# Kernel tuning notes

Hardware: AMD Instinct MI355X
Metric: run time of the kernel (lower is better)

The kernel has to match this reference:

```python
import jax, jax.numpy as jnp
import numpy as np

B, S, IN, H, OUT = 512, 1024, 32, 128, 1


def setup_inputs() -> dict:
    key = jax.random.key(0)
    ks = jax.random.split(key, 7)
    sc = 1.0 / np.sqrt(H)  # torch LSTM/Linear default init scale
    return {
        "x": jax.random.normal(ks[0], (B, S, IN), dtype=jnp.float32),
        "W_ih": jax.random.normal(ks[1], (4 * H, IN), dtype=jnp.float32) * sc,
        "W_hh": jax.random.normal(ks[2], (4 * H, H), dtype=jnp.float32) * sc,
        "b_ih": jax.random.normal(ks[3], (4 * H,), dtype=jnp.float32) * sc,
        "b_hh": jax.random.normal(ks[4], (4 * H,), dtype=jnp.float32) * sc,
        "W_lin": jax.random.normal(ks[5], (OUT, H * S), dtype=jnp.float32) * (1.0 / np.sqrt(H * S)),
        "b_lin": jax.random.normal(ks[6], (OUT,), dtype=jnp.float32) * (1.0 / np.sqrt(H * S)),
    }


def _lstm(x, W_ih, W_hh, b_ih, b_hh):
    # x: [B,S,IN]. Precompute input projection for all timesteps (one big GEMM).
    xw = jnp.einsum("bsi,gi->bsg", x, W_ih) + (b_ih + b_hh)  # [B,S,4H]
    h0 = jnp.zeros((x.shape[0], W_hh.shape[1]), dtype=x.dtype)
    c0 = jnp.zeros_like(h0)

    def step(carry, xw_t):
        h, c = carry
        gates = xw_t + h @ W_hh.T  # [B,4H]
        i, f, g, o = jnp.split(gates, 4, axis=-1)  # torch gate order i,f,g,o
        i = jax.nn.sigmoid(i)
        f = jax.nn.sigmoid(f)
        g = jnp.tanh(g)
        o = jax.nn.sigmoid(o)
        c = f * c + i * g
        h = o * jnp.tanh(c)
        return (h, c), h

    (_, _), hs = jax.lax.scan(step, (h0, c0), jnp.swapaxes(xw, 0, 1))  # hs: [S,B,H]
    return jnp.swapaxes(hs, 0, 1)  # [B,S,H]


def reference(x, W_ih, W_hh, b_ih, b_hh, W_lin, b_lin):
    lstm_out = _lstm(x, W_ih, W_hh, b_ih, b_hh)          # [B,S,H]
    flat = lstm_out.reshape(lstm_out.shape[0], -1)        # [B,S*H]
    return flat @ W_lin.T + b_lin                         # [B,OUT]
```

## Files before the change

### kernel.cpp

```cpp
#include <hip/hip_runtime.h>

constexpr int B = 512, S = 1024, IN = 32, H = 128;
constexpr int KTOT = IN + H;
constexpr int KSL = KTOT / 4;

template <int CTRL>
__device__ __forceinline__ float dpp_qp(float v) {
  return __int_as_float(__builtin_amdgcn_update_dpp(
      0, __float_as_int(v), CTRL, 0xF, 0xF, true));
}
__device__ __forceinline__ float sigm(float v) {
  float e = __builtin_amdgcn_exp2f(-1.4426950408889634f * v);
  return __builtin_amdgcn_rcpf(1.0f + e);
}
__device__ __forceinline__ float tanh_(float v) {
  float e = __builtin_amdgcn_exp2f(-2.8853900817779268f * v);
  return 2.0f * __builtin_amdgcn_rcpf(1.0f + e) - 1.0f;
}

__global__ __launch_bounds__(512, 2)
void lstm_fused(const float* __restrict__ x, const float* __restrict__ Wih,
                const float* __restrict__ Whh, const float* __restrict__ bih,
                const float* __restrict__ bhh, const float* __restrict__ Wlin,
                const float* __restrict__ blin, float* __restrict__ out) {
  __shared__ alignas(16) float hxA[KTOT];
  __shared__ alignas(16) float hxB[KTOT];
  __shared__ float red[2 * H];

  const int tid = threadIdx.x;
  const int g = tid >> 2;
  const int j = tid & 3;
  const int b0 = blockIdx.x * 2;

  float w[4][KSL];
#pragma unroll
  for (int c = 0; c < 4; ++c) {
    const int n = c * H + g;
#pragma unroll
    for (int kk = 0; kk < KSL; ++kk) {
      const int k = KSL * j + kk;
      const float* p = (k < IN) ? (Wih + n * IN + k) : (Whh + n * H + (k - IN));
      w[c][kk] = *p;
    }
  }
  float bias[4];
#pragma unroll
  for (int c = 0; c < 4; ++c) bias[c] = bih[c * H + g] + bhh[c * H + g];

  if (tid < KTOT) { hxA[tid] = 0.0f; hxB[tid] = 0.0f; }
  __syncthreads();
  if (tid < 2 * IN) {
    const int b = tid >> 5, k = tid & 31;
    (b ? hxB : hxA)[k] = x[(size_t)(b0 + b) * (S * IN) + k];
  }
  __syncthreads();

  float cc0 = 0.f, cc1 = 0.f;
  float oa0 = 0.f, oa1 = 0.f;
  const int xb = g >> 5, xk = g & 31;

  for (int s = 0; s < S; ++s) {
    float wl = 0.f, xn = 0.f;
    if (j == 0) wl = Wlin[s * H + g];
    const bool xload = (j == 1) && (g < 64) && (s + 1 < S);
    if (xload) xn = x[(size_t)(b0 + xb) * (S * IN) + (s + 1) * IN + xk];

    float acc[4][2];
#pragma unroll
    for (int c = 0; c < 4; ++c) { acc[c][0] = 0.f; acc[c][1] = 0.f; }
    const float4* pA = reinterpret_cast<const float4*>(hxA + KSL * j);
    const float4* pB = reinterpret_cast<const float4*>(hxB + KSL * j);
#pragma unroll
    for (int q = 0; q < KSL / 4; ++q) {
      const float4 va = pA[q];
      const float4 vb = pB[q];
      const float ea[4] = {va.x, va.y, va.z, va.w};
      const float eb[4] = {vb.x, vb.y, vb.z, vb.w};
#pragma unroll
      for (int u = 0; u < 4; ++u)
#pragma unroll
        for (int c = 0; c < 4; ++c) {
          acc[c][0] = fmaf(ea[u], w[c][4 * q + u], acc[c][0]);
          acc[c][1] = fmaf(eb[u], w[c][4 * q + u], acc[c][1]);
        }
    }
#pragma unroll
    for (int c = 0; c < 4; ++c)
#pragma unroll
      for (int b = 0; b < 2; ++b) {
        float v = acc[c][b];
        v += dpp_qp<0xB1>(v);
        v += dpp_qp<0x4E>(v);
        acc[c][b] = v;
      }
    __syncthreads();
    if (j == 0) {
#pragma unroll
      for (int b = 0; b < 2; ++b) {
        const float gi = sigm(acc[0][b] + bias[0]);
        const float gf = sigm(acc[1][b] + bias[1]);
        const float gc = tanh_(acc[2][b] + bias[2]);
        const float go = sigm(acc[3][b] + bias[3]);
        float& cc = b ? cc1 : cc0;
        cc = gf * cc + gi * gc;
        const float h = go * tanh_(cc);
        (b ? hxB : hxA)[IN + g] = h;
        (b ? oa1 : oa0) += h * wl;
      }
    } else if (xload) {
      (xb ? hxB : hxA)[xk] = xn;
    }
    __syncthreads();
  }

  if (j == 0) { red[2 * g] = oa0; red[2 * g + 1] = oa1; }
  __syncthreads();
  if (tid < 2) {
    float sum = blin[0];
    for (int k = 0; k < H; ++k) sum += red[2 * k + tid];
    out[b0 + tid] = sum;
  }
}

extern "C" void kernel_launch(void* const* d_in, const int* in_sizes, int n_in,
                              void* d_out, int out_size, void* d_ws, size_t ws_size,
                              hipStream_t stream) {
  const float* x    = (const float*)d_in[0];
  const float* Wih  = (const float*)d_in[1];
  const float* Whh  = (const float*)d_in[2];
  const float* bih  = (const float*)d_in[3];
  const float* bhh  = (const float*)d_in[4];
  const float* Wlin = (const float*)d_in[5];
  const float* blin = (const float*)d_in[6];
  float* outp = (float*)d_out;
  hipLaunchKernelGGL(lstm_fused, dim3(B / 2), dim3(512), 0, stream,
                     x, Wih, Whh, bih, bhh, Wlin, blin, outp);
}
```

Baseline: 1.351 ms.

## Use fp16 dot2 for recurrent matvec with double-buffered hidden state

Converts weights and the shared h/x vector to fp16 and uses v_dot2_f32_f16 with fp32 accumulation, halving the FMA count and the weight register footprint. The shared state is double-buffered by timestep parity, which removes one of the two barriers per step. The gate nonlinearity work is now split so lanes j=0 and j=1 each handle one batch row, instead of lane 0 doing both. The risk is fp16 rounding error on the weights and hidden state accumulating over 1024 recurrent steps.

```diff
diff --git a/kernel.cpp b/kernel.cpp
--- a/kernel.cpp
+++ b/kernel.cpp
@@ -1,13 +1,20 @@
 #include <hip/hip_runtime.h>
+#include <stdint.h>
 
 constexpr int B = 512, S = 1024, IN = 32, H = 128;
 constexpr int KTOT = IN + H;
 constexpr int KSL = KTOT / 4;
+constexpr int KP = KSL / 2;
+
+typedef uint32_t u32;
 
 template <int CTRL>
 __device__ __forceinline__ float dpp_qp(float v) {
   return __int_as_float(__builtin_amdgcn_update_dpp(
       0, __float_as_int(v), CTRL, 0xF, 0xF, true));
+}
+__device__ __forceinline__ void dot2(float& c, u32 a, u32 b) {
+  asm("v_dot2_f32_f16 %0, %1, %2, %0" : "+v"(c) : "v"(a), "v"(b));
 }
 __device__ __forceinline__ float sigm(float v) {
   float e = __builtin_amdgcn_exp2f(-1.4426950408889634f * v);
@@ -23,8 +30,7 @@
                 const float* __restrict__ Whh, const float* __restrict__ bih,
                 const float* __restrict__ bhh, const float* __restrict__ Wlin,
                 const float* __restrict__ blin, float* __restrict__ out) {
-  __shared__ alignas(16) float hxA[KTOT];
-  __shared__ alignas(16) float hxB[KTOT];
+  __shared__ alignas(16) _Float16 hx[2][2][KTOT];
   __shared__ float red[2 * H];
 
   const int tid = threadIdx.x;
@@ -32,57 +38,66 @@
   const int j = tid & 3;
   const int b0 = blockIdx.x * 2;
 
-  float w[4][KSL];
+  u32 w[4][KP];
 #pragma unroll
   for (int c = 0; c < 4; ++c) {
     const int n = c * H + g;
 #pragma unroll
-    for (int kk = 0; kk < KSL; ++kk) {
-      const int k = KSL * j + kk;
-      const float* p = (k < IN) ? (Wih + n * IN + k) : (Whh + n * H + (k - IN));
-      w[c][kk] = *p;
+    for (int p = 0; p < KP; ++p) {
+      const int k0 = KSL * j + 2 * p;
+      const int k1 = k0 + 1;
+      const float f0 = (k0 < IN) ? Wih[n * IN + k0] : Whh[n * H + (k0 - IN)];
+      const float f1 = (k1 < IN) ? Wih[n * IN + k1] : Whh[n * H + (k1 - IN)];
+      union { _Float16 h[2]; u32 u; } cv;
+      cv.h[0] = (_Float16)f0;
+      cv.h[1] = (_Float16)f1;
+      w[c][p] = cv.u;
     }
   }
+#pragma unroll
+  for (int c = 0; c < 4; ++c)
+#pragma unroll
+    for (int p = 0; p < KP; ++p) asm volatile("" : "+v"(w[c][p]));
+
   float bias[4];
 #pragma unroll
   for (int c = 0; c < 4; ++c) bias[c] = bih[c * H + g] + bhh[c * H + g];
 
-  if (tid < KTOT) { hxA[tid] = 0.0f; hxB[tid] = 0.0f; }
+  if (tid < 2 * KTOT) ((_Float16*)hx)[tid] = (_Float16)0.0f;
   __syncthreads();
   if (tid < 2 * IN) {
     const int b = tid >> 5, k = tid & 31;
-    (b ? hxB : hxA)[k] = x[(size_t)(b0 + b) * (S * IN) + k];
+    hx[0][b][k] = (_Float16)x[(size_t)(b0 + b) * (S * IN) + k];
   }
   __syncthreads();
 
-  float cc0 = 0.f, cc1 = 0.f;
-  float oa0 = 0.f, oa1 = 0.f;
+  float cc = 0.f;
+  float oa = 0.f;
   const int xb = g >> 5, xk = g & 31;
+  const int bb = j & 1;
 
   for (int s = 0; s < S; ++s) {
+    const int p = s & 1, np = p ^ 1;
     float wl = 0.f, xn = 0.f;
-    if (j == 0) wl = Wlin[s * H + g];
-    const bool xload = (j == 1) && (g < 64) && (s + 1 < S);
+    if (j < 2) wl = Wlin[s * H + g];
+    const bool xload = (j == 2) && (g < 64) && (s + 1 < S);
     if (xload) xn = x[(size_t)(b0 + xb) * (S * IN) + (s + 1) * IN + xk];
 
     float acc[4][2];
 #pragma unroll
     for (int c = 0; c < 4; ++c) { acc[c][0] = 0.f; acc[c][1] = 0.f; }
-    const float4* pA = reinterpret_cast<const float4*>(hxA + KSL * j);
-    const float4* pB = reinterpret_cast<const float4*>(hxB + KSL * j);
 #pragma unroll
-    for (int q = 0; q < KSL / 4; ++q) {
-      const float4 va = pA[q];
-      const float4 vb = pB[q];
-      const float ea[4] = {va.x, va.y, va.z, va.w};
-      const float eb[4] = {vb.x, vb.y, vb.z, vb.w};
+    for (int b = 0; b < 2; ++b) {
+      const uint4* pp = reinterpret_cast<const uint4*>(&hx[p][b][KSL * j]);
 #pragma unroll
-      for (int u = 0; u < 4; ++u)
+      for (int q = 0; q < 5; ++q) {
+        const uint4 v = pp[q];
+        const u32 e[4] = {v.x, v.y, v.z, v.w};
 #pragma unroll
-        for (int c = 0; c < 4; ++c) {
-          acc[c][0] = fmaf(ea[u], w[c][4 * q + u], acc[c][0]);
-          acc[c][1] = fmaf(eb[u], w[c][4 * q + u], acc[c][1]);
-        }
+        for (int u = 0; u < 4; ++u)
+#pragma unroll
+          for (int c = 0; c < 4; ++c) dot2(acc[c][b], e[u], w[c][4 * q + u]);
+      }
     }
 #pragma unroll
     for (int c = 0; c < 4; ++c)
@@ -93,31 +108,26 @@
         v += dpp_qp<0x4E>(v);
         acc[c][b] = v;
       }
-    __syncthreads();
-    if (j == 0) {
-#pragma unroll
-      for (int b = 0; b < 2; ++b) {
-        const float gi = sigm(acc[0][b] + bias[0]);
-        const float gf = sigm(acc[1][b] + bias[1]);
-        const float gc = tanh_(acc[2][b] + bias[2]);
-        const float go = sigm(acc[3][b] + bias[3]);
-        float& cc = b ? cc1 : cc0;
-        cc = gf * cc + gi * gc;
-        const float h = go * tanh_(cc);
-        (b ? hxB : hxA)[IN + g] = h;
-        (b ? oa1 : oa0) += h * wl;
-      }
+    const float gi = sigm(acc[0][bb] + bias[0]);
+    const float gf = sigm(acc[1][bb] + bias[1]);
+    const float gg = tanh_(acc[2][bb] + bias[2]);
+    const float go = sigm(acc[3][bb] + bias[3]);
+    cc = gf * cc + gi * gg;
+    const float h = go * tanh_(cc);
+    if (j < 2) {
+      hx[np][bb][IN + g] = (_Float16)h;
+      oa += h * wl;
     } else if (xload) {
-      (xb ? hxB : hxA)[xk] = xn;
+      hx[np][xb][xk] = (_Float16)xn;
     }
     __syncthreads();
   }
 
-  if (j == 0) { red[2 * g] = oa0; red[2 * g + 1] = oa1; }
+  if (j < 2) red[j * H + g] = oa;
   __syncthreads();
   if (tid < 2) {
     float sum = blin[0];
-    for (int k = 0; k < H; ++k) sum += red[2 * k + tid];
+    for (int k = 0; k < H; ++k) sum += red[tid * H + k];
     out[b0 + tid] = sum;
   }
 }
```

New measurement: 1.473 ms. 9.0% more time.
